# Kernel tuning notes

Hardware: AMD Instinct MI355X
Metric: run time of the kernel (lower is better)

The kernel has to match this reference:

```python
import jax, jax.numpy as jnp
import numpy as np
import math

B, S, D = 2, 2048, 2048
H, KVH, HD = 16, 8, 128  # n_heads, n_kv_heads, head_dim
N_REP = H // KVH
ROPE_THETA = 500000.0
NEG_INF = -1e9


def _rope(t, f):
    # t: (B,S,nh,HD) viewed as pairs; f: (S,HD//2,2) = (cos,sin)
    tp = t.reshape(*t.shape[:-1], HD // 2, 2)          # (B,S,nh,HD//2,2)
    fb = f[:, None]                                     # (S,1,HD//2,2)
    row1 = (tp * fb).sum(-1)                            # x0*c + x1*s
    f_rot = jnp.stack([fb[..., 1], -fb[..., 0]], axis=-1)  # (s, -c)
    row0 = (tp * f_rot).sum(-1)                         # x0*s - x1*c
    return jnp.stack([row0, row1], axis=-1).reshape(t.shape)


def setup_inputs() -> dict:
    key = jax.random.key(0)
    ks = jax.random.split(key, 5)
    x = jax.random.normal(ks[0], (B, S, D), dtype=jnp.float32)
    # RoPE table: (S, HD//2, 2) stacked (cos, sin)
    inv_freq = 1.0 / (ROPE_THETA ** (np.arange(0, HD, 2, dtype=np.float32) / HD))
    t = np.arange(S, dtype=np.float32)
    ang = np.outer(t, inv_freq)                         # (S, HD//2)
    freqs_cis = jnp.asarray(np.stack([np.cos(ang), np.sin(ang)], axis=-1))
    # causal additive mask (S,S)
    mask = jnp.where(jnp.triu(jnp.ones((S, S), dtype=bool), k=1), NEG_INF, 0.0).astype(jnp.float32)
    sc = 1.0 / math.sqrt(D)
    wq = jax.random.normal(ks[1], (D, H * HD), dtype=jnp.float32) * sc
    wk = jax.random.normal(ks[2], (D, KVH * HD), dtype=jnp.float32) * sc
    wv = jax.random.normal(ks[3], (D, KVH * HD), dtype=jnp.float32) * sc
    wo = jax.random.normal(ks[4], (H * HD, D), dtype=jnp.float32) * sc
    return {"x": x, "freqs_cis": freqs_cis, "mask": mask, "wq": wq, "wk": wk, "wv": wv, "wo": wo}


def reference(x, freqs_cis, mask, wq, wk, wv, wo):
    bsz, seqlen, _ = x.shape
    xq = (x @ wq).reshape(bsz, seqlen, H, HD)
    xk = (x @ wk).reshape(bsz, seqlen, KVH, HD)
    xv = (x @ wv).reshape(bsz, seqlen, KVH, HD)
    xq = _rope(xq, freqs_cis)
    xk = _rope(xk, freqs_cis)
    keys = jnp.repeat(xk, N_REP, axis=2)                # (B,S,H,HD)
    values = jnp.repeat(xv, N_REP, axis=2)
    q = xq.transpose(0, 2, 1, 3)                        # (B,H,S,HD)
    k = keys.transpose(0, 2, 1, 3)
    v = values.transpose(0, 2, 1, 3)
    scores = jnp.einsum('bhqd,bhkd->bhqk', q, k) / math.sqrt(HD)
    scores = scores + mask                              # broadcast (S,S)
    probs = jax.nn.softmax(scores.astype(jnp.float32), axis=-1).astype(q.dtype)
    out = jnp.einsum('bhqk,bhkd->bhqd', probs, v)
    out = out.transpose(0, 2, 1, 3).reshape(bsz, seqlen, H * HD)
    return out @ wo
```

## Files before the change

kernel.cpp:

```cpp
#include <hip/hip_runtime.h>

typedef short short8 __attribute__((ext_vector_type(8)));
typedef float v4f __attribute__((ext_vector_type(4)));
typedef float v16f __attribute__((ext_vector_type(16)));

#define LOG2E 1.4426950408889634f

__device__ __forceinline__ unsigned short f2bf(float f) {
  unsigned int u = __float_as_uint(f);
  u += 0x7fff + ((u >> 16) & 1);
  return (unsigned short)(u >> 16);
}
__device__ __forceinline__ float b2f(unsigned short h) {
  return __uint_as_float(((unsigned int)h) << 16);
}
__device__ __forceinline__ void gl_lds16(const void* g, void* l) {
  __builtin_amdgcn_global_load_lds((const __attribute__((address_space(1))) void*)g,
                                   (__attribute__((address_space(3))) void*)l, 16, 0, 0);
}

__global__ __launch_bounds__(256) void cvt_f32_bf16(const float* __restrict__ src,
                                                    unsigned short* __restrict__ dst, int n) {
  int i = (blockIdx.x * 256 + threadIdx.x) * 4;
  if (i < n) {
    float4 v = *(const float4*)(src + i);
    ushort4 o;
    o.x = f2bf(v.x); o.y = f2bf(v.y); o.z = f2bf(v.z); o.w = f2bf(v.w);
    *(ushort4*)(dst + i) = o;
  }
}

__global__ __launch_bounds__(256) void transpose_f32_bf16(const float* __restrict__ src,
                                                          unsigned short* __restrict__ dst,
                                                          int srcCols) {
  __shared__ float tile[64][65];
  const int c0 = blockIdx.x * 64;
  const int r0 = blockIdx.y * 64;
  const int t = threadIdx.x;
#pragma unroll
  for (int i = 0; i < 16; ++i) {
    int idx = t + i * 256; int r = idx >> 6, c = idx & 63;
    tile[r][c] = src[(size_t)(r0 + r) * srcCols + c0 + c];
  }
  __syncthreads();
#pragma unroll
  for (int i = 0; i < 16; ++i) {
    int idx = t + i * 256; int r = idx >> 6, c = idx & 63;
    dst[(size_t)(c0 + r) * 2048 + r0 + c] = f2bf(tile[c][r]);
  }
}

template <bool OUT_BF16>
__global__ __launch_bounds__(256) void gemm_bt(const unsigned short* __restrict__ A,
                                               const unsigned short* __restrict__ Bt,
                                               void* __restrict__ Cv,
                                               int M, int N, int K) {
  __shared__ __align__(16) unsigned short As[2][128 * 32];
  __shared__ __align__(16) unsigned short Bs[2][128 * 32];
  const int t = threadIdx.x;
  const int wave = t >> 6, lane = t & 63, quad = lane >> 4, l16 = lane & 15;
  const int tm = blockIdx.y * 128, tn = blockIdx.x * 128;
  const int wm = (wave >> 1) * 64, wn = (wave & 1) * 64;
  v4f acc[4][4];
#pragma unroll
  for (int i = 0; i < 4; ++i)
#pragma unroll
    for (int j = 0; j < 4; ++j) acc[i][j] = (v4f){0.f, 0.f, 0.f, 0.f};

  const int swz = (l16 >> 1) & 3;

  const int s0 = t, s1 = 256 + t;
  const unsigned short* pa0 = A + (size_t)(tm + (s0 >> 2)) * K + ((s0 & 3) ^ ((s0 >> 3) & 3)) * 8;
  const unsigned short* pa1 = A + (size_t)(tm + (s1 >> 2)) * K + ((s1 & 3) ^ ((s1 >> 3) & 3)) * 8;
  const unsigned short* pb0 = Bt + (size_t)(tn + (s0 >> 2)) * K + ((s0 & 3) ^ ((s0 >> 3) & 3)) * 8;
  const unsigned short* pb1 = Bt + (size_t)(tn + (s1 >> 2)) * K + ((s1 & 3) ^ ((s1 >> 3) & 3)) * 8;
  const int dOff0 = (wave * 64) * 8;
  const int dOff1 = (256 + wave * 64) * 8;

  gl_lds16(pa0, &As[0][dOff0]); gl_lds16(pa1, &As[0][dOff1]);
  gl_lds16(pb0, &Bs[0][dOff0]); gl_lds16(pb1, &Bs[0][dOff1]);
  pa0 += 32; pa1 += 32; pb0 += 32; pb1 += 32;

  const int nit = K >> 5;
  for (int it = 0; it < nit; ++it) {
    __syncthreads();
    const int cur = it & 1;
    if (it + 1 < nit) {
      const int nxt = cur ^ 1;
      gl_lds16(pa0, &As[nxt][dOff0]); gl_lds16(pa1, &As[nxt][dOff1]);
      gl_lds16(pb0, &Bs[nxt][dOff0]); gl_lds16(pb1, &Bs[nxt][dOff1]);
      pa0 += 32; pa1 += 32; pb0 += 32; pb1 += 32;
    }
    short8 af[4], bf[4];
#pragma unroll
    for (int mt = 0; mt < 4; ++mt)
      af[mt] = *(const short8*)(&As[cur][(wm + mt * 16 + l16) * 32 + (quad ^ swz) * 8]);
#pragma unroll
    for (int nt = 0; nt < 4; ++nt)
      bf[nt] = *(const short8*)(&Bs[cur][(wn + nt * 16 + l16) * 32 + (quad ^ swz) * 8]);
#pragma unroll
    for (int mt = 0; mt < 4; ++mt)
#pragma unroll
      for (int nt = 0; nt < 4; ++nt)
        acc[mt][nt] = __builtin_amdgcn_mfma_f32_16x16x32_bf16(af[mt], bf[nt], acc[mt][nt], 0, 0, 0);
  }

#pragma unroll
  for (int mt = 0; mt < 4; ++mt)
#pragma unroll
    for (int nt = 0; nt < 4; ++nt)
#pragma unroll
      for (int r = 0; r < 4; ++r) {
        int row = tm + wm + mt * 16 + quad * 4 + r;
        int col = tn + wn + nt * 16 + l16;
        float v = acc[mt][nt][r];
        if (OUT_BF16) ((unsigned short*)Cv)[(size_t)row * N + col] = f2bf(v);
        else          ((float*)Cv)[(size_t)row * N + col] = v;
      }
}

template <bool OUT_BF16>
__global__ __launch_bounds__(512, 2) void gemm256(const unsigned short* __restrict__ A,
                                                  const unsigned short* __restrict__ Bt,
                                                  void* __restrict__ Cv,
                                                  int M, int N, int K) {
  __shared__ __align__(16) unsigned short As[2][256 * 64];
  __shared__ __align__(16) unsigned short Bs[2][256 * 64];
  const int t = threadIdx.x;
  const int wave = t >> 6, lane = t & 63, quad = lane >> 4, l16 = lane & 15;
  const int wr = wave >> 2, wc = wave & 3;

  const int gx = N >> 8;
  int id = blockIdx.y * gridDim.x + blockIdx.x;
  const int nwg = gridDim.x * gridDim.y;
  id = (id & 7) * (nwg >> 3) + (id >> 3);
  const int tm = (id / gx) << 8, tn = (id % gx) << 8;

  v4f acc[8][4];
#pragma unroll
  for (int i = 0; i < 8; ++i)
#pragma unroll
    for (int j = 0; j < 4; ++j) acc[i][j] = (v4f){0.f, 0.f, 0.f, 0.f};

  const int s0 = t, s1 = 512 + t;
  const size_t hA = (size_t)128 * K;
  const unsigned short* a0 = A + (size_t)(tm + (s0 >> 3)) * K + ((s0 & 7) ^ ((s0 >> 3) & 7)) * 8;
  const unsigned short* a1 = A + (size_t)(tm + (s1 >> 3)) * K + ((s1 & 7) ^ ((s1 >> 3) & 7)) * 8;
  const unsigned short* b0 = Bt + (size_t)(tn + (s0 >> 3)) * K + ((s0 & 7) ^ ((s0 >> 3) & 7)) * 8;
  const unsigned short* b1 = Bt + (size_t)(tn + (s1 >> 3)) * K + ((s1 & 7) ^ ((s1 >> 3) & 7)) * 8;
  const int d0 = (wave * 64) * 8;
  const int d1 = (512 + wave * 64) * 8;

#define STG_A(buf, h, koff)                                         \
  do {                                                              \
    gl_lds16(a0 + (size_t)(h) * hA + (koff), &As[buf][(h) * 8192 + d0]); \
    gl_lds16(a1 + (size_t)(h) * hA + (koff), &As[buf][(h) * 8192 + d1]); \
  } while (0)
#define STG_B(buf, h, koff)                                         \
  do {                                                              \
    gl_lds16(b0 + (size_t)(h) * hA + (koff), &Bs[buf][(h) * 8192 + d0]); \
    gl_lds16(b1 + (size_t)(h) * hA + (koff), &Bs[buf][(h) * 8192 + d1]); \
  } while (0)

  const int aBase = (wr * 128 + l16) * 64;
  const int bBase = (wc * 64 + l16) * 64;
  const int c0 = (quad ^ (l16 & 7)) * 8;
  const int c1 = ((4 + quad) ^ (l16 & 7)) * 8;

  const int nkt = K >> 6;

  STG_A(0, 0, 0); STG_A(0, 1, 0);
  STG_B(0, 0, 0); STG_B(0, 1, 0);
  STG_B(1, 0, 64); STG_A(1, 0, 64);
  asm volatile("s_waitcnt vmcnt(4)" ::: "memory");
  __builtin_amdgcn_s_barrier();

  short8 af[4][2], bf[4][2];
  for (int kt = 0; kt < nkt; ++kt) {
    const int cur = kt & 1, nxt = cur ^ 1;
    const int koff = kt << 6;

#pragma unroll
    for (int m = 0; m < 4; ++m) {
      af[m][0] = *(const short8*)(&As[cur][aBase + m * 1024 + c0]);
      af[m][1] = *(const short8*)(&As[cur][aBase + m * 1024 + c1]);
    }
#pragma unroll
    for (int n = 0; n < 2; ++n) {
      bf[n][0] = *(const short8*)(&Bs[cur][bBase + n * 1024 + c0]);
      bf[n][1] = *(const short8*)(&Bs[cur][bBase + n * 1024 + c1]);
    }
    if (kt + 1 < nkt) { STG_A(nxt, 1, koff + 64); STG_B(nxt, 1, koff + 64); }
    __builtin_amdgcn_s_barrier();
    asm volatile("s_waitcnt lgkmcnt(0)" ::: "memory");
    __builtin_amdgcn_s_setprio(1);
#pragma unroll
    for (int m = 0; m < 4; ++m)
#pragma unroll
      for (int n = 0; n < 2; ++n) {
        acc[m][n] = __builtin_amdgcn_mfma_f32_16x16x32_bf16(af[m][0], bf[n][0], acc[m][n], 0, 0, 0);
        acc[m][n] = __builtin_amdgcn_mfma_f32_16x16x32_bf16(af[m][1], bf[n][1], acc[m][n], 0, 0, 0);
      }
    __builtin_amdgcn_s_setprio(0);
    __builtin_amdgcn_s_barrier();

#pragma unroll
    for (int n = 2; n < 4; ++n) {
      bf[n][0] = *(const short8*)(&Bs[cur][bBase + n * 1024 + c0]);
      bf[n][1] = *(const short8*)(&Bs[cur][bBase + n * 1024 + c1]);
    }
    __builtin_amdgcn_s_barrier();
    asm volatile("s_waitcnt lgkmcnt(0)" ::: "memory");
    __builtin_amdgcn_s_setprio(1);
#pragma unroll
    for (int m = 0; m < 4; ++m)
#pragma unroll
      for (int n = 2; n < 4; ++n) {
        acc[m][n] = __builtin_amdgcn_mfma_f32_16x16x32_bf16(af[m][0], bf[n][0], acc[m][n], 0, 0, 0);
        acc[m][n] = __builtin_amdgcn_mfma_f32_16x16x32_bf16(af[m][1], bf[n][1], acc[m][n], 0, 0, 0);
      }
    __builtin_amdgcn_s_setprio(0);
    __builtin_amdgcn_s_barrier();

#pragma unroll
    for (int m = 0; m < 4; ++m) {
      af[m][0] = *(const short8*)(&As[cur][aBase + (4 + m) * 1024 + c0]);
      af[m][1] = *(const short8*)(&As[cur][aBase + (4 + m) * 1024 + c1]);
    }
    if (kt + 2 < nkt) STG_B(cur, 0, koff + 128);
    __builtin_amdgcn_s_barrier();
    asm volatile("s_waitcnt lgkmcnt(0)" ::: "memory");
    __builtin_amdgcn_s_setprio(1);
#pragma unroll
    for (int m = 0; m < 4; ++m)
#pragma unroll
      for (int n = 0; n < 2; ++n) {
        acc[4 + m][n] = __builtin_amdgcn_mfma_f32_16x16x32_bf16(af[m][0], bf[n][0], acc[4 + m][n], 0, 0, 0);
        acc[4 + m][n] = __builtin_amdgcn_mfma_f32_16x16x32_bf16(af[m][1], bf[n][1], acc[4 + m][n], 0, 0, 0);
      }
    __builtin_amdgcn_s_setprio(0);
    __builtin_amdgcn_s_barrier();

    if (kt + 2 < nkt) {
      STG_A(cur, 0, koff + 128);
      asm volatile("s_waitcnt vmcnt(4)" ::: "memory");
    } else {
      asm volatile("s_waitcnt vmcnt(0)" ::: "memory");
    }
    __builtin_amdgcn_s_barrier();
    __builtin_amdgcn_s_setprio(1);
#pragma unroll
    for (int m = 0; m < 4; ++m)
#pragma unroll
      for (int n = 2; n < 4; ++n) {
        acc[4 + m][n] = __builtin_amdgcn_mfma_f32_16x16x32_bf16(af[m][0], bf[n][0], acc[4 + m][n], 0, 0, 0);
        acc[4 + m][n] = __builtin_amdgcn_mfma_f32_16x16x32_bf16(af[m][1], bf[n][1], acc[4 + m][n], 0, 0, 0);
      }
    __builtin_amdgcn_s_setprio(0);
    __builtin_amdgcn_s_barrier();
  }
#undef STG_A
#undef STG_B

#pragma unroll
  for (int mf = 0; mf < 8; ++mf)
#pragma unroll
    for (int nf = 0; nf < 4; ++nf)
#pragma unroll
      for (int r = 0; r < 4; ++r) {
        int row = tm + wr * 128 + mf * 16 + quad * 4 + r;
        int col = tn + wc * 64 + nf * 16 + l16;
        float v = acc[mf][nf][r];
        if (OUT_BF16) ((unsigned short*)Cv)[(size_t)row * N + col] = f2bf(v);
        else          ((float*)Cv)[(size_t)row * N + col] = v;
      }
}

__global__ __launch_bounds__(256) void rope_k(unsigned short* __restrict__ qkv,
                                              const float* __restrict__ freqs) {
  const int bs = blockIdx.x;
  const int s = bs & 2047;
  const float qscale = 0.08838834764831845f;
  unsigned int* row = (unsigned int*)(qkv + (size_t)bs * 4096);
  const float2* fr2 = (const float2*)(freqs + s * 128);
#pragma unroll
  for (int k = 0; k < 6; ++k) {
    int d = threadIdx.x + k * 256;
    float sc = (d < 1024) ? qscale : 1.0f;
    float2 cs = fr2[d & 63];
    unsigned int w = row[d];
    float x0 = b2f((unsigned short)(w & 0xffffu));
    float x1 = b2f((unsigned short)(w >> 16));
    float y0 = (x0 * cs.y - x1 * cs.x) * sc;
    float y1 = (x0 * cs.x + x1 * cs.y) * sc;
    row[d] = ((unsigned int)f2bf(y1) << 16) | (unsigned int)f2bf(y0);
  }
}

__global__ __launch_bounds__(256) void transpose_v(const unsigned short* __restrict__ qkv,
                                                   unsigned short* __restrict__ vt) {
  __shared__ unsigned short tile[64][65];
  const int s0 = blockIdx.x * 64, d0 = blockIdx.y * 64;
  const int bk = blockIdx.z; const int b = bk >> 3, kv = bk & 7;
  const int t = threadIdx.x;
#pragma unroll
  for (int i = 0; i < 16; ++i) {
    int idx = t + i * 256; int r = idx >> 6, c = idx & 63;
    tile[r][c] = qkv[(size_t)(b * 2048 + s0 + r) * 4096 + 3072 + kv * 128 + d0 + c];
  }
  __syncthreads();
#pragma unroll
  for (int i = 0; i < 16; ++i) {
    int idx = t + i * 256; int r = idx >> 6, c = idx & 63;
    vt[((size_t)bk * 128 + d0 + r) * 2048 + s0 + c] = tile[c][r];
  }
}

__global__ __launch_bounds__(256, 1) void attn_k(const unsigned short* __restrict__ qkv,
                                                 const unsigned short* __restrict__ vt,
                                                 unsigned short* __restrict__ Ob) {
  __shared__ __align__(16) unsigned short Ks[2][128 * 128];
  __shared__ __align__(16) unsigned short Vs[2][128 * 128];
  const int t = threadIdx.x, wave = t >> 6, lane = t & 63;
  const int l31 = lane & 31, hh2 = lane >> 5;
  const int jp = blockIdx.x, hd = blockIdx.y, b = blockIdx.z;
  const int kv = hd >> 1;

  auto stage = [&](int jt, int buf) {
#pragma unroll
    for (int issue = 0; issue < 8; ++issue) {
      int s = issue * 256 + t;
      int row = s >> 4;
      int src = ((s & 15) ^ (row & 15)) * 8;
      gl_lds16(qkv + (size_t)(b * 2048 + jt * 128 + row) * 4096 + 2048 + kv * 128 + src,
               &Ks[buf][(issue * 256 + wave * 64) * 8]);
      gl_lds16(vt + ((size_t)(b * 8 + kv) * 128 + row) * 2048 + jt * 128 + src,
               &Vs[buf][(issue * 256 + wave * 64) * 8]);
    }
  };

  for (int pass = 0; pass < 2; ++pass) {
    const int qblk = (pass == 0) ? jp : 15 - jp;
    const int q0 = qblk * 128;
    const int qrel = wave * 32 + l31;
    const int qrow = q0 + qrel;

    short8 qf[8];
    {
      const unsigned short* qp = qkv + (size_t)(b * 2048 + qrow) * 4096 + hd * 128 + hh2 * 8;
#pragma unroll
      for (int ks = 0; ks < 8; ++ks) qf[ks] = *(const short8*)(qp + ks * 16);
    }
    stage(0, 0);

    v16f oa[4];
#pragma unroll
    for (int i = 0; i < 4; ++i)
#pragma unroll
      for (int r = 0; r < 16; ++r) oa[i][r] = 0.f;
    float m_s = -3.0e38f, l_s = 0.f;

    const int ntl = qblk + 1;
    for (int jt = 0; jt < ntl; ++jt) {
      const int cur = jt & 1;
      if (jt + 1 < ntl) {
        stage(jt + 1, cur ^ 1);
        asm volatile("s_waitcnt vmcnt(16)" ::: "memory");
      } else {
        asm volatile("s_waitcnt vmcnt(0)" ::: "memory");
      }
      __builtin_amdgcn_s_barrier();

      v16f st[4];
#pragma unroll
      for (int i = 0; i < 4; ++i)
#pragma unroll
        for (int r = 0; r < 16; ++r) st[i][r] = 0.f;
#pragma unroll
      for (int ks = 0; ks < 8; ++ks)
#pragma unroll
        for (int kt = 0; kt < 4; ++kt) {
          int row = kt * 32 + l31;
          short8 kf = *(const short8*)(
              &Ks[cur][row * 128 + (((ks * 2 + hh2) ^ (row & 15)) * 8)]);
          st[kt] = __builtin_amdgcn_mfma_f32_32x32x16_bf16(kf, qf[ks], st[kt], 0, 0, 0);
        }

      float mx = -3.0e38f;
      if (jt == qblk) {
#pragma unroll
        for (int kt = 0; kt < 4; ++kt)
#pragma unroll
          for (int r = 0; r < 16; ++r) {
            int key = kt * 32 + (r & 3) + 8 * (r >> 2) + 4 * hh2;
            float v = st[kt][r];
            if (key > qrel) v = -1.0e30f;
            st[kt][r] = v;
            mx = fmaxf(mx, v);
          }
      } else {
#pragma unroll
        for (int kt = 0; kt < 4; ++kt)
#pragma unroll
          for (int r = 0; r < 16; ++r) mx = fmaxf(mx, st[kt][r]);
      }
      mx = fmaxf(mx, __shfl_xor(mx, 32));

      if (__ballot(mx > m_s + 8.0f)) {
        float mn = fmaxf(m_s, mx);
        float alpha = exp2f((m_s - mn) * LOG2E);
        m_s = mn;
#pragma unroll
        for (int i = 0; i < 4; ++i)
#pragma unroll
          for (int r = 0; r < 16; ++r) oa[i][r] *= alpha;
        l_s *= alpha;
      }

      float lt = 0.f;
      unsigned int PD[4][8];
#pragma unroll
      for (int kt = 0; kt < 4; ++kt)
#pragma unroll
        for (int j = 0; j < 8; ++j) {
          float p0 = exp2f((st[kt][2 * j]     - m_s) * LOG2E);
          float p1 = exp2f((st[kt][2 * j + 1] - m_s) * LOG2E);
          lt += p0 + p1;
          unsigned int pd;
          asm("v_cvt_pk_bf16_f32 %0, %1, %2" : "=v"(pd) : "v"(p0), "v"(p1));
          PD[kt][j] = pd;
        }
      lt += __shfl_xor(lt, 32);
      l_s += lt;

      unsigned int XD[4][8];
#pragma unroll
      for (int kt = 0; kt < 4; ++kt)
#pragma unroll
        for (int j = 0; j < 8; ++j) XD[kt][j] = __shfl_xor(PD[kt][j], 32);

#pragma unroll
      for (int ks = 0; ks < 8; ++ks) {
        const int tt = ks >> 1, w4 = (ks & 1) * 4;
        union { unsigned int u[4]; short8 s8; } pf;
        pf.u[0] = hh2 ? XD[tt][w4 + 2] : PD[tt][w4 + 0];
        pf.u[1] = hh2 ? XD[tt][w4 + 3] : PD[tt][w4 + 1];
        pf.u[2] = hh2 ? PD[tt][w4 + 2] : XD[tt][w4 + 0];
        pf.u[3] = hh2 ? PD[tt][w4 + 3] : XD[tt][w4 + 1];
#pragma unroll
        for (int dt = 0; dt < 4; ++dt) {
          int row = dt * 32 + l31;
          short8 vf = *(const short8*)(
              &Vs[cur][row * 128 + (((ks * 2 + hh2) ^ (row & 15)) * 8)]);
          oa[dt] = __builtin_amdgcn_mfma_f32_32x32x16_bf16(vf, pf.s8, oa[dt], 0, 0, 0);
        }
      }
      __builtin_amdgcn_s_barrier();
    }

    float inv = 1.0f / l_s;
    unsigned short* orow = Ob + (size_t)(b * 2048 + qrow) * 2048 + hd * 128;
#pragma unroll
    for (int dt = 0; dt < 4; ++dt)
#pragma unroll
      for (int g = 0; g < 4; ++g) {
        ushort4 wv;
        wv.x = f2bf(oa[dt][4 * g + 0] * inv);
        wv.y = f2bf(oa[dt][4 * g + 1] * inv);
        wv.z = f2bf(oa[dt][4 * g + 2] * inv);
        wv.w = f2bf(oa[dt][4 * g + 3] * inv);
        *(ushort4*)(orow + dt * 32 + 8 * g + 4 * hh2) = wv;
      }
    __syncthreads();
  }
}

extern "C" void kernel_launch(void* const* d_in, const int* in_sizes, int n_in,
                              void* d_out, int out_size, void* d_ws, size_t ws_size,
                              hipStream_t stream) {
  (void)in_sizes; (void)n_in; (void)out_size; (void)ws_size;
  const float* x  = (const float*)d_in[0];
  const float* fr = (const float*)d_in[1];
  const float* wq = (const float*)d_in[3];
  const float* wk = (const float*)d_in[4];
  const float* wv = (const float*)d_in[5];
  const float* wo = (const float*)d_in[6];
  float* out = (float*)d_out;

  char* ws = (char*)d_ws;
  unsigned short* Xb    = (unsigned short*)(ws);
  unsigned short* WqkvT = (unsigned short*)(ws + (size_t)(16u << 20));
  unsigned short* WoT   = (unsigned short*)(ws + (size_t)(32u << 20));
  unsigned short* QKV   = (unsigned short*)(ws + (size_t)(40u << 20));
  unsigned short* Vt    = (unsigned short*)(ws);
  unsigned short* Ob    = (unsigned short*)(ws + (size_t)(16u << 20));

  cvt_f32_bf16<<<8192, 256, 0, stream>>>(x, Xb, 2 * 2048 * 2048);
  transpose_f32_bf16<<<dim3(32, 32), 256, 0, stream>>>(wq, WqkvT, 2048);
  transpose_f32_bf16<<<dim3(16, 32), 256, 0, stream>>>(wk, WqkvT + (size_t)2048 * 2048, 1024);
  transpose_f32_bf16<<<dim3(16, 32), 256, 0, stream>>>(wv, WqkvT + (size_t)3072 * 2048, 1024);
  transpose_f32_bf16<<<dim3(32, 32), 256, 0, stream>>>(wo, WoT, 2048);
  gemm256<true><<<dim3(16, 16), 512, 0, stream>>>(Xb, WqkvT, QKV, 4096, 4096, 2048);
  rope_k<<<4096, 256, 0, stream>>>(QKV, fr);
  transpose_v<<<dim3(32, 2, 16), 256, 0, stream>>>(QKV, Vt);
  attn_k<<<dim3(8, 16, 2), 256, 0, stream>>>(QKV, Vt, Ob);
  gemm_bt<false><<<dim3(16, 32), 256, 0, stream>>>(Ob, WoT, out, 4096, 2048, 2048);
}
```

Baseline: 363.5 us.

## Halve attention KV tile to allow two blocks per CU, one q-block per block

The attention kernel now stages 64-key K/V tiles instead of 128, halving LDS per block so two blocks can be resident per CU (launch bounds 2). The paired-pass load balancing (each block doing q-block j and 15-j) is replaced by one q-block per block with a grid of 16x16x2, launching heaviest blocks first. The max and sum reductions are split into two accumulators to shorten dependency chains. It trades more loop iterations and barriers per key, plus register pressure under the tighter launch bound, for higher occupancy and better latency hiding.

After: 369.3 us. About the same (+1.6%).

```diff
diff --git a/kernel.cpp b/kernel.cpp
--- a/kernel.cpp
+++ b/kernel.cpp
@@ -316,163 +316,170 @@
   }
 }
 
-__global__ __launch_bounds__(256, 1) void attn_k(const unsigned short* __restrict__ qkv,
+__global__ __launch_bounds__(256, 2) void attn_k(const unsigned short* __restrict__ qkv,
                                                  const unsigned short* __restrict__ vt,
                                                  unsigned short* __restrict__ Ob) {
-  __shared__ __align__(16) unsigned short Ks[2][128 * 128];
-  __shared__ __align__(16) unsigned short Vs[2][128 * 128];
+  __shared__ __align__(16) unsigned short Ks[2][64 * 128];
+  __shared__ __align__(16) unsigned short Vs[2][128 * 64];
   const int t = threadIdx.x, wave = t >> 6, lane = t & 63;
   const int l31 = lane & 31, hh2 = lane >> 5;
-  const int jp = blockIdx.x, hd = blockIdx.y, b = blockIdx.z;
+  const int qblk = 15 - blockIdx.x;
+  const int hd = blockIdx.y, b = blockIdx.z;
   const int kv = hd >> 1;
+  const int q0 = qblk * 128;
+  const int qrel = wave * 32 + l31;
+  const int qrow = q0 + qrel;
 
   auto stage = [&](int jt, int buf) {
 #pragma unroll
-    for (int issue = 0; issue < 8; ++issue) {
+    for (int issue = 0; issue < 4; ++issue) {
       int s = issue * 256 + t;
       int row = s >> 4;
       int src = ((s & 15) ^ (row & 15)) * 8;
-      gl_lds16(qkv + (size_t)(b * 2048 + jt * 128 + row) * 4096 + 2048 + kv * 128 + src,
+      gl_lds16(qkv + (size_t)(b * 2048 + jt * 64 + row) * 4096 + 2048 + kv * 128 + src,
                &Ks[buf][(issue * 256 + wave * 64) * 8]);
-      gl_lds16(vt + ((size_t)(b * 8 + kv) * 128 + row) * 2048 + jt * 128 + src,
+    }
+#pragma unroll
+    for (int issue = 0; issue < 4; ++issue) {
+      int s = issue * 256 + t;
+      int row = s >> 3;
+      int src = ((s & 7) ^ (row & 7)) * 8;
+      gl_lds16(vt + ((size_t)(b * 8 + kv) * 128 + row) * 2048 + jt * 64 + src,
                &Vs[buf][(issue * 256 + wave * 64) * 8]);
     }
   };
 
-  for (int pass = 0; pass < 2; ++pass) {
-    const int qblk = (pass == 0) ? jp : 15 - jp;
-    const int q0 = qblk * 128;
-    const int qrel = wave * 32 + l31;
-    const int qrow = q0 + qrel;
-
-    short8 qf[8];
-    {
-      const unsigned short* qp = qkv + (size_t)(b * 2048 + qrow) * 4096 + hd * 128 + hh2 * 8;
-#pragma unroll
-      for (int ks = 0; ks < 8; ++ks) qf[ks] = *(const short8*)(qp + ks * 16);
-    }
-    stage(0, 0);
-
-    v16f oa[4];
-#pragma unroll
-    for (int i = 0; i < 4; ++i)
-#pragma unroll
-      for (int r = 0; r < 16; ++r) oa[i][r] = 0.f;
-    float m_s = -3.0e38f, l_s = 0.f;
-
-    const int ntl = qblk + 1;
-    for (int jt = 0; jt < ntl; ++jt) {
-      const int cur = jt & 1;
-      if (jt + 1 < ntl) {
-        stage(jt + 1, cur ^ 1);
-        asm volatile("s_waitcnt vmcnt(16)" ::: "memory");
-      } else {
-        asm volatile("s_waitcnt vmcnt(0)" ::: "memory");
-      }
-      __builtin_amdgcn_s_barrier();
-
-      v16f st[4];
+  short8 qf[8];
+  {
+    const unsigned short* qp = qkv + (size_t)(b * 2048 + qrow) * 4096 + hd * 128 + hh2 * 8;
+#pragma unroll
+    for (int ks = 0; ks < 8; ++ks) qf[ks] = *(const short8*)(qp + ks * 16);
+  }
+  stage(0, 0);
+
+  v16f oa[4];
+#pragma unroll
+  for (int i = 0; i < 4; ++i)
+#pragma unroll
+    for (int r = 0; r < 16; ++r) oa[i][r] = 0.f;
+  float m_s = -3.0e38f, l_s = 0.f;
+
+  const int ntl = 2 * (qblk + 1);
+  for (int jt = 0; jt < ntl; ++jt) {
+    const int cur = jt & 1;
+    if (jt + 1 < ntl) {
+      stage(jt + 1, cur ^ 1);
+      asm volatile("s_waitcnt vmcnt(8)" ::: "memory");
+    } else {
+      asm volatile("s_waitcnt vmcnt(0)" ::: "memory");
+    }
+    __builtin_amdgcn_s_barrier();
+
+    v16f st[2];
+#pragma unroll
+    for (int i = 0; i < 2; ++i)
+#pragma unroll
+      for (int r = 0; r < 16; ++r) st[i][r] = 0.f;
+#pragma unroll
+    for (int ks = 0; ks < 8; ++ks)
+#pragma unroll
+      for (int kt = 0; kt < 2; ++kt) {
+        int row = kt * 32 + l31;
+        short8 kf = *(const short8*)(
+            &Ks[cur][row * 128 + (((ks * 2 + hh2) ^ (row & 15)) * 8)]);
+        st[kt] = __builtin_amdgcn_mfma_f32_32x32x16_bf16(kf, qf[ks], st[kt], 0, 0, 0);
+      }
+
+    float mx0 = -3.0e38f, mx1 = -3.0e38f;
+    if (jt >= 2 * qblk) {
+      const int rel = qrel - (jt * 64 - q0);
+#pragma unroll
+      for (int kt = 0; kt < 2; ++kt)
+#pragma unroll
+        for (int r = 0; r < 16; ++r) {
+          int key = kt * 32 + (r & 3) + 8 * (r >> 2) + 4 * hh2;
+          float v = st[kt][r];
+          if (key > rel) v = -1.0e30f;
+          st[kt][r] = v;
+          if (r & 1) mx1 = fmaxf(mx1, v); else mx0 = fmaxf(mx0, v);
+        }
+    } else {
+#pragma unroll
+      for (int kt = 0; kt < 2; ++kt)
+#pragma unroll
+        for (int r = 0; r < 16; ++r) {
+          if (r & 1) mx1 = fmaxf(mx1, st[kt][r]); else mx0 = fmaxf(mx0, st[kt][r]);
+        }
+    }
+    float mx = fmaxf(mx0, mx1);
+    mx = fmaxf(mx, __shfl_xor(mx, 32));
+
+    if (__ballot(mx > m_s + 8.0f)) {
+      float mn = fmaxf(m_s, mx);
+      float alpha = exp2f((m_s - mn) * LOG2E);
+      m_s = mn;
 #pragma unroll
       for (int i = 0; i < 4; ++i)
 #pragma unroll
-        for (int r = 0; r < 16; ++r) st[i][r] = 0.f;
-#pragma unroll
-      for (int ks = 0; ks < 8; ++ks)
-#pragma unroll
-        for (int kt = 0; kt < 4; ++kt) {
-          int row = kt * 32 + l31;
-          short8 kf = *(const short8*)(
-              &Ks[cur][row * 128 + (((ks * 2 + hh2) ^ (row & 15)) * 8)]);
-          st[kt] = __builtin_amdgcn_mfma_f32_32x32x16_bf16(kf, qf[ks], st[kt], 0, 0, 0);
-        }
-
-      float mx = -3.0e38f;
-      if (jt == qblk) {
-#pragma unroll
-        for (int kt = 0; kt < 4; ++kt)
-#pragma unroll
-          for (int r = 0; r < 16; ++r) {
-            int key = kt * 32 + (r & 3) + 8 * (r >> 2) + 4 * hh2;
-            float v = st[kt][r];
-            if (key > qrel) v = -1.0e30f;
-            st[kt][r] = v;
-            mx = fmaxf(mx, v);
-          }
-      } else {
-#pragma unroll
-        for (int kt = 0; kt < 4; ++kt)
-#pragma unroll
-          for (int r = 0; r < 16; ++r) mx = fmaxf(mx, st[kt][r]);
-      }
-      mx = fmaxf(mx, __shfl_xor(mx, 32));
-
-      if (__ballot(mx > m_s + 8.0f)) {
-        float mn = fmaxf(m_s, mx);
-        float alpha = exp2f((m_s - mn) * LOG2E);
-        m_s = mn;
-#pragma unroll
-        for (int i = 0; i < 4; ++i)
-#pragma unroll
-          for (int r = 0; r < 16; ++r) oa[i][r] *= alpha;
-        l_s *= alpha;
-      }
-
-      float lt = 0.f;
-      unsigned int PD[4][8];
-#pragma unroll
-      for (int kt = 0; kt < 4; ++kt)
-#pragma unroll
-        for (int j = 0; j < 8; ++j) {
-          float p0 = exp2f((st[kt][2 * j]     - m_s) * LOG2E);
-          float p1 = exp2f((st[kt][2 * j + 1] - m_s) * LOG2E);
-          lt += p0 + p1;
-          unsigned int pd;
-          asm("v_cvt_pk_bf16_f32 %0, %1, %2" : "=v"(pd) : "v"(p0), "v"(p1));
-          PD[kt][j] = pd;
-        }
-      lt += __shfl_xor(lt, 32);
-      l_s += lt;
-
-      unsigned int XD[4][8];
-#pragma unroll
-      for (int kt = 0; kt < 4; ++kt)
-#pragma unroll
-        for (int j = 0; j < 8; ++j) XD[kt][j] = __shfl_xor(PD[kt][j], 32);
-
-#pragma unroll
-      for (int ks = 0; ks < 8; ++ks) {
-        const int tt = ks >> 1, w4 = (ks & 1) * 4;
-        union { unsigned int u[4]; short8 s8; } pf;
-        pf.u[0] = hh2 ? XD[tt][w4 + 2] : PD[tt][w4 + 0];
-        pf.u[1] = hh2 ? XD[tt][w4 + 3] : PD[tt][w4 + 1];
-        pf.u[2] = hh2 ? PD[tt][w4 + 2] : XD[tt][w4 + 0];
-        pf.u[3] = hh2 ? PD[tt][w4 + 3] : XD[tt][w4 + 1];
-#pragma unroll
-        for (int dt = 0; dt < 4; ++dt) {
-          int row = dt * 32 + l31;
-          short8 vf = *(const short8*)(
-              &Vs[cur][row * 128 + (((ks * 2 + hh2) ^ (row & 15)) * 8)]);
-          oa[dt] = __builtin_amdgcn_mfma_f32_32x32x16_bf16(vf, pf.s8, oa[dt], 0, 0, 0);
-        }
-      }
-      __builtin_amdgcn_s_barrier();
-    }
-
-    float inv = 1.0f / l_s;
-    unsigned short* orow = Ob + (size_t)(b * 2048 + qrow) * 2048 + hd * 128;
-#pragma unroll
-    for (int dt = 0; dt < 4; ++dt)
-#pragma unroll
-      for (int g = 0; g < 4; ++g) {
-        ushort4 wv;
-        wv.x = f2bf(oa[dt][4 * g + 0] * inv);
-        wv.y = f2bf(oa[dt][4 * g + 1] * inv);
-        wv.z = f2bf(oa[dt][4 * g + 2] * inv);
-        wv.w = f2bf(oa[dt][4 * g + 3] * inv);
-        *(ushort4*)(orow + dt * 32 + 8 * g + 4 * hh2) = wv;
-      }
-    __syncthreads();
-  }
+        for (int r = 0; r < 16; ++r) oa[i][r] *= alpha;
+      l_s *= alpha;
+    }
+
+    float lt0 = 0.f, lt1 = 0.f;
+    unsigned int PD[2][8];
+#pragma unroll
+    for (int kt = 0; kt < 2; ++kt)
+#pragma unroll
+      for (int j = 0; j < 8; ++j) {
+        float p0 = exp2f((st[kt][2 * j]     - m_s) * LOG2E);
+        float p1 = exp2f((st[kt][2 * j + 1] - m_s) * LOG2E);
+        lt0 += p0; lt1 += p1;
+        unsigned int pd;
+        asm("v_cvt_pk_bf16_f32 %0, %1, %2" : "=v"(pd) : "v"(p0), "v"(p1));
+        PD[kt][j] = pd;
+      }
+    float lt = lt0 + lt1;
+    lt += __shfl_xor(lt, 32);
+    l_s += lt;
+
+    unsigned int XD[2][8];
+#pragma unroll
+    for (int kt = 0; kt < 2; ++kt)
+#pragma unroll
+      for (int j = 0; j < 8; ++j) XD[kt][j] = __shfl_xor(PD[kt][j], 32);
+
+#pragma unroll
+    for (int ks = 0; ks < 4; ++ks) {
+      const int tt = ks >> 1, w4 = (ks & 1) * 4;
+      union { unsigned int u[4]; short8 s8; } pf;
+      pf.u[0] = hh2 ? XD[tt][w4 + 2] : PD[tt][w4 + 0];
+      pf.u[1] = hh2 ? XD[tt][w4 + 3] : PD[tt][w4 + 1];
+      pf.u[2] = hh2 ? PD[tt][w4 + 2] : XD[tt][w4 + 0];
+      pf.u[3] = hh2 ? PD[tt][w4 + 3] : XD[tt][w4 + 1];
+#pragma unroll
+      for (int dt = 0; dt < 4; ++dt) {
+        int row = dt * 32 + l31;
+        short8 vf = *(const short8*)(
+            &Vs[cur][row * 64 + (((ks * 2 + hh2) ^ (row & 7)) * 8)]);
+        oa[dt] = __builtin_amdgcn_mfma_f32_32x32x16_bf16(vf, pf.s8, oa[dt], 0, 0, 0);
+      }
+    }
+    __builtin_amdgcn_s_barrier();
+  }
+
+  float inv = 1.0f / l_s;
+  unsigned short* orow = Ob + (size_t)(b * 2048 + qrow) * 2048 + hd * 128;
+#pragma unroll
+  for (int dt = 0; dt < 4; ++dt)
+#pragma unroll
+    for (int g = 0; g < 4; ++g) {
+      ushort4 wv;
+      wv.x = f2bf(oa[dt][4 * g + 0] * inv);
+      wv.y = f2bf(oa[dt][4 * g + 1] * inv);
+      wv.z = f2bf(oa[dt][4 * g + 2] * inv);
+      wv.w = f2bf(oa[dt][4 * g + 3] * inv);
+      *(ushort4*)(orow + dt * 32 + 8 * g + 4 * hh2) = wv;
+    }
 }
 
 extern "C" void kernel_launch(void* const* d_in, const int* in_sizes, int n_in,
@@ -503,6 +510,6 @@
   gemm256<true><<<dim3(16, 16), 512, 0, stream>>>(Xb, WqkvT, QKV, 4096, 4096, 2048);
   rope_k<<<4096, 256, 0, stream>>>(QKV, fr);
   transpose_v<<<dim3(32, 2, 16), 256, 0, stream>>>(QKV, Vt);
-  attn_k<<<dim3(8, 16, 2), 256, 0, stream>>>(QKV, Vt, Ob);
+  attn_k<<<dim3(16, 16, 2), 256, 0, stream>>>(QKV, Vt, Ob);
   gemm_bt<false><<<dim3(16, 32), 256, 0, stream>>>(Ob, WoT, out, 4096, 2048, 2048);
 }
```
